# Kernel optimization log

Measured on AMD Instinct MI355X. Metric: run time of the kernel, lower is better.

The kernel has to match this reference:

```python
import jax, jax.numpy as jnp
import numpy as np

B, S, E, H = 2, 2048, 2048, 16
D = E // H  # head_dim = 128
ROPE_BASE = 10000.0


def _rope_tables(seq_len, dim, dtype):
    inv_freq = 1.0 / (ROPE_BASE ** (jnp.arange(0, dim, 2, dtype=jnp.float32) / dim))
    pos = jnp.arange(seq_len, dtype=jnp.float32)
    freqs = jnp.outer(pos, inv_freq)            # [S, D/2]
    emb = jnp.concatenate([freqs, freqs], -1)    # [S, D]
    return jnp.cos(emb).astype(dtype), jnp.sin(emb).astype(dtype)


def _rotate_half(x):
    x1, x2 = jnp.split(x, 2, axis=-1)
    return jnp.concatenate([-x2, x1], axis=-1)


def _apply_rope(x, cos, sin):
    # x: [B,H,S,D]; cos/sin: [S,D] broadcast over batch+heads
    return x * cos[None, None] + _rotate_half(x) * sin[None, None]


def setup_inputs() -> dict:
    key = jax.random.key(0)
    k1, k2, k3 = jax.random.split(key, 3)
    x = jax.random.normal(k1, (B, S, E), dtype=jnp.float32)
    w_qkv = jax.random.normal(k2, (3 * E, E), dtype=jnp.float32) * (E ** -0.5)
    w_out = jax.random.normal(k3, (E, E), dtype=jnp.float32) * (E ** -0.5)
    return {"x": x, "w_qkv": w_qkv, "w_out": w_out}


def reference(x, w_qkv, w_out):
    b, s, e = x.shape
    qkv = x @ w_qkv.T                                # [B,S,3E]
    q, k, v = jnp.split(qkv, 3, axis=-1)
    def to_heads(t):
        return t.reshape(b, s, H, D).transpose(0, 2, 1, 3)  # [B,H,S,D]
    q, k, v = to_heads(q), to_heads(k), to_heads(v)
    cos, sin = _rope_tables(s, D, x.dtype)
    q = _apply_rope(q, cos, sin)
    k = _apply_rope(k, cos, sin)
    scale = 1.0 / jnp.sqrt(jnp.asarray(D, x.dtype))
    scores = jnp.einsum('bhqd,bhkd->bhqk', q, k) * scale
    causal = jnp.tril(jnp.ones((s, s), dtype=bool))
    scores = jnp.where(causal[None, None], scores, jnp.asarray(-jnp.inf, scores.dtype))
    attn = jax.nn.softmax(scores, axis=-1)
    y = jnp.einsum('bhqk,bhkd->bhqd', attn, v)       # [B,H,S,D]
    y = y.transpose(0, 2, 1, 3).reshape(b, s, e)
    return y @ w_out.T
```

## Files before the change

### kernel.cpp

```cpp
#include <hip/hip_runtime.h>
#include <stdint.h>

constexpr int BATCH = 2;
constexpr int SEQ   = 2048;
constexpr int EMB   = 2048;
constexpr int NH    = 16;
constexpr int HD    = 128;
constexpr int QKV3  = 3 * EMB;

typedef unsigned short u16;
typedef __attribute__((ext_vector_type(8))) short bf16x8;
typedef __attribute__((ext_vector_type(4))) float floatx4;

__device__ inline float bf2f(u16 u) {
  union { unsigned int i; float f; } v; v.i = ((unsigned int)u) << 16; return v.f;
}
__device__ inline u16 f2bf(float f) {
  union { float f; unsigned int i; } v; v.f = f;
  unsigned int x = v.i;
  return (u16)((x + 0x7fffu + ((x >> 16) & 1u)) >> 16);
}

__device__ inline void load_lds16(const void* g, void* l) {
  __builtin_amdgcn_global_load_lds((const __attribute__((address_space(1))) unsigned int*)g,
                                   (__attribute__((address_space(3))) unsigned int*)l,
                                   16, 0, 0);
}

__device__ inline void block_barrier() {
  __builtin_amdgcn_sched_barrier(0);
  asm volatile("" ::: "memory");
  __builtin_amdgcn_s_barrier();
  asm volatile("" ::: "memory");
  __builtin_amdgcn_sched_barrier(0);
}

__global__ void cvt_f32_bf16(const float* __restrict__ src, u16* __restrict__ dst, int n4) {
  const int i = blockIdx.x * blockDim.x + threadIdx.x;
  if (i < n4) {
    const float4 v = ((const float4*)src)[i];
    ushort4 o;
    o.x = f2bf(v.x); o.y = f2bf(v.y); o.z = f2bf(v.z); o.w = f2bf(v.w);
    ((ushort4*)dst)[i] = o;
  }
}

constexpr int BM = 128, BN = 128, BK = 32;

template <bool F32OUT>
__global__ __launch_bounds__(256) void gemm_bt(const u16* __restrict__ A,
                                               const u16* __restrict__ Bm,
                                               u16* __restrict__ Cb,
                                               float* __restrict__ Cf,
                                               int M, int N, int K) {
  __shared__ __align__(16) u16 As[BM * BK];
  __shared__ __align__(16) u16 Bs[BN * BK];
  const int tid  = threadIdx.x;
  const int wave = tid >> 6, lane = tid & 63;
  const int wm = (wave & 1) * 64, wn = (wave >> 1) * 64;
  const int m0 = blockIdx.y * BM, n0 = blockIdx.x * BN;

  floatx4 acc[4][4];
#pragma unroll
  for (int i = 0; i < 4; ++i)
#pragma unroll
    for (int j = 0; j < 4; ++j) acc[i][j] = {0.f, 0.f, 0.f, 0.f};

  const int lrow = lane >> 2;
  const int lcol = (lane & 3) * 8;
  const int frow = lane & 15;
  const int fk   = (lane >> 4) * 8;

  for (int kt = 0; kt < K; kt += BK) {
#pragma unroll
    for (int inst = 0; inst < 2; ++inst) {
      const int rbase = wave * 32 + inst * 16;
      load_lds16(A  + (size_t)(m0 + rbase + lrow) * K + kt + lcol, &As[rbase * BK]);
      load_lds16(Bm + (size_t)(n0 + rbase + lrow) * K + kt + lcol, &Bs[rbase * BK]);
    }
    asm volatile("s_waitcnt vmcnt(0)" ::: "memory");
    __syncthreads();

    bf16x8 af[4], bfr[4];
#pragma unroll
    for (int mi = 0; mi < 4; ++mi)
      af[mi] = *(const bf16x8*)&As[(wm + mi * 16 + frow) * BK + fk];
#pragma unroll
    for (int ni = 0; ni < 4; ++ni)
      bfr[ni] = *(const bf16x8*)&Bs[(wn + ni * 16 + frow) * BK + fk];
#pragma unroll
    for (int mi = 0; mi < 4; ++mi)
#pragma unroll
      for (int ni = 0; ni < 4; ++ni)
        acc[mi][ni] = __builtin_amdgcn_mfma_f32_16x16x32_bf16(af[mi], bfr[ni], acc[mi][ni], 0, 0, 0);
    __syncthreads();
  }

  const int crow0 = (lane >> 4) * 4;
  const int ccol  = lane & 15;
#pragma unroll
  for (int mi = 0; mi < 4; ++mi)
#pragma unroll
    for (int ni = 0; ni < 4; ++ni) {
      const int row = m0 + wm + mi * 16 + crow0;
      const int col = n0 + wn + ni * 16 + ccol;
#pragma unroll
      for (int r = 0; r < 4; ++r) {
        const size_t off = (size_t)(row + r) * N + col;
        if (F32OUT) Cf[off] = acc[mi][ni][r];
        else        Cb[off] = f2bf(acc[mi][ni][r]);
      }
    }
}

__global__ __launch_bounds__(512, 2) void gemm_bt192(const u16* __restrict__ A,
                                                     const u16* __restrict__ Bm,
                                                     u16* __restrict__ Cb,
                                                     int M, int N, int K) {
  __shared__ __align__(16) u16 sh[57344];
  char* ldsb = (char*)sh;

  const int tid  = threadIdx.x;
  const int wave = tid >> 6, lane = tid & 63;
  const int wrow = wave >> 1;
  const int wcol = wave & 1;
  const int m0 = blockIdx.y * 256, n0 = blockIdx.x * 192;
  const int frow = lane & 15, quad = lane >> 4;
  const int KT = K >> 6;

  const int srow8 = tid >> 3;
  const int scolE = (((tid & 7) ^ (srow8 & 7)) << 3);
  auto stageA = [&](int t, int d, int a) {
    const int r = a * 64 + srow8;
    load_lds16(A + (size_t)(m0 + r) * K + t * 64 + scolE,
               ldsb + d * 57344 + a * 8192 + wave * 1024);
  };
  auto stageB = [&](int t, int d, int bi) {
    const int r = bi * 64 + srow8;
    load_lds16(Bm + (size_t)(n0 + r) * K + t * 64 + scolE,
               ldsb + d * 57344 + 32768 + bi * 8192 + wave * 1024);
  };

  floatx4 acc[4][6];
#pragma unroll
  for (int i = 0; i < 4; ++i)
#pragma unroll
    for (int j = 0; j < 6; ++j) acc[i][j] = {0.f, 0.f, 0.f, 0.f};

#pragma unroll
  for (int a = 0; a < 4; ++a) stageA(0, 0, a);
#pragma unroll
  for (int bi = 0; bi < 3; ++bi) stageB(0, 0, bi);

  for (int t = 0; t < KT; ++t) {
    const int d = t & 1, dn = d ^ 1;
    const char* dbuf = ldsb + d * 57344;
    const bool pf = (t + 1 < KT);

    if (pf) {
      stageA(t + 1, dn, 0); stageA(t + 1, dn, 1); stageA(t + 1, dn, 2);
      asm volatile("s_waitcnt vmcnt(3)" ::: "memory");
    } else {
      asm volatile("s_waitcnt vmcnt(0)" ::: "memory");
    }
    block_barrier();

    bf16x8 af[4][2], bf0[2][2];
#pragma unroll
    for (int mi = 0; mi < 4; ++mi) {
      const int ra = wrow * 64 + mi * 16 + frow;
#pragma unroll
      for (int kk = 0; kk < 2; ++kk) {
        const int cb = (kk * 64 + quad * 16) ^ ((ra & 7) << 4);
        af[mi][kk] = *(const bf16x8*)(dbuf + ra * 128 + cb);
      }
    }
#pragma unroll
    for (int ni = 0; ni < 2; ++ni) {
      const int rb = wcol * 96 + ni * 16 + frow;
#pragma unroll
      for (int kk = 0; kk < 2; ++kk) {
        const int cb = (kk * 64 + quad * 16) ^ ((rb & 7) << 4);
        bf0[ni][kk] = *(const bf16x8*)(dbuf + 32768 + rb * 128 + cb);
      }
    }
    asm volatile("s_waitcnt lgkmcnt(0)" ::: "memory");
    __builtin_amdgcn_sched_barrier(0);
    __builtin_amdgcn_s_setprio(1);
#pragma unroll
    for (int mi = 0; mi < 4; ++mi)
#pragma unroll
      for (int ni = 0; ni < 2; ++ni)
#pragma unroll
        for (int kk = 0; kk < 2; ++kk)
          acc[mi][ni] = __builtin_amdgcn_mfma_f32_16x16x32_bf16(af[mi][kk], bf0[ni][kk], acc[mi][ni], 0, 0, 0);
    __builtin_amdgcn_s_setprio(0);
    block_barrier();

    bf16x8 bf1[2][2];
#pragma unroll
    for (int ni = 0; ni < 2; ++ni) {
      const int rb = wcol * 96 + (2 + ni) * 16 + frow;
#pragma unroll
      for (int kk = 0; kk < 2; ++kk) {
        const int cb = (kk * 64 + quad * 16) ^ ((rb & 7) << 4);
        bf1[ni][kk] = *(const bf16x8*)(dbuf + 32768 + rb * 128 + cb);
      }
    }
    if (pf) { stageA(t + 1, dn, 3); stageB(t + 1, dn, 0); }
    block_barrier();
    asm volatile("s_waitcnt lgkmcnt(0)" ::: "memory");
    __builtin_amdgcn_sched_barrier(0);
    __builtin_amdgcn_s_setprio(1);
#pragma unroll
    for (int mi = 0; mi < 4; ++mi)
#pragma unroll
      for (int ni = 0; ni < 2; ++ni)
#pragma unroll
        for (int kk = 0; kk < 2; ++kk)
          acc[mi][2 + ni] = __builtin_amdgcn_mfma_f32_16x16x32_bf16(af[mi][kk], bf1[ni][kk], acc[mi][2 + ni], 0, 0, 0);
    __builtin_amdgcn_s_setprio(0);
    block_barrier();

    bf16x8 bf2[2][2];
#pragma unroll
    for (int ni = 0; ni < 2; ++ni) {
      const int rb = wcol * 96 + (4 + ni) * 16 + frow;
#pragma unroll
      for (int kk = 0; kk < 2; ++kk) {
        const int cb = (kk * 64 + quad * 16) ^ ((rb & 7) << 4);
        bf2[ni][kk] = *(const bf16x8*)(dbuf + 32768 + rb * 128 + cb);
      }
    }
    if (pf) { stageB(t + 1, dn, 1); stageB(t + 1, dn, 2); }
    block_barrier();
    asm volatile("s_waitcnt lgkmcnt(0)" ::: "memory");
    __builtin_amdgcn_sched_barrier(0);
    __builtin_amdgcn_s_setprio(1);
#pragma unroll
    for (int mi = 0; mi < 4; ++mi)
#pragma unroll
      for (int ni = 0; ni < 2; ++ni)
#pragma unroll
        for (int kk = 0; kk < 2; ++kk)
          acc[mi][4 + ni] = __builtin_amdgcn_mfma_f32_16x16x32_bf16(af[mi][kk], bf2[ni][kk], acc[mi][4 + ni], 0, 0, 0);
    __builtin_amdgcn_s_setprio(0);
    block_barrier();
  }

#pragma unroll
  for (int mi = 0; mi < 4; ++mi)
#pragma unroll
    for (int ni = 0; ni < 6; ++ni) {
      const int row = m0 + wrow * 64 + mi * 16 + quad * 4;
      const int col = n0 + wcol * 96 + ni * 16 + frow;
#pragma unroll
      for (int r = 0; r < 4; ++r)
        Cb[(size_t)(row + r) * N + col] = f2bf(acc[mi][ni][r]);
    }
}

__global__ void rope_inplace(u16* __restrict__ qkv) {
  const int t   = blockIdx.x * blockDim.x + threadIdx.x;
  const int j   = t & 63;
  const int idx = t >> 6;
  const int h   = idx & (NH - 1);
  const int bs  = idx >> 4;
  const int s   = bs & (SEQ - 1);

  u16* base = qkv + (size_t)bs * QKV3 + h * HD;

  const float inv_freq = exp2f(-(float)j * (13.287712379549449f / 64.0f));
  const float ang = (float)s * inv_freq;
  const float c = cosf(ang), sn = sinf(ang);

#pragma unroll
  for (int part = 0; part < 2; ++part) {
    u16* p = base + part * EMB;
    const float x1 = bf2f(p[j]), x2 = bf2f(p[j + 64]);
    p[j]      = f2bf(x1 * c - x2 * sn);
    p[j + 64] = f2bf(x2 * c + x1 * sn);
  }
}

__global__ __launch_bounds__(256) void transpose_v(const u16* __restrict__ qkv,
                                                   u16* __restrict__ VT) {
  __shared__ u16 vtile[64][136];
  const int tid = threadIdx.x;
  const int s0 = blockIdx.x * 64;
  const int bh = blockIdx.y;
  const int b = bh >> 4, h = bh & 15;

  const u16* Vp = qkv + (size_t)b * SEQ * QKV3 + 2 * EMB + h * HD;
  {
    const int r = tid >> 2, cp = (tid & 3) * 32;
    const uint4* src = (const uint4*)(Vp + (size_t)(s0 + r) * QKV3 + cp);
    uint4* dst = (uint4*)&vtile[r][cp];
    dst[0] = src[0]; dst[1] = src[1]; dst[2] = src[2]; dst[3] = src[3];
  }
  __syncthreads();
  {
    const int d = tid >> 1, ck = (tid & 1) * 32;
    ushort4 o[8];
#pragma unroll
    for (int i = 0; i < 8; ++i) {
      o[i].x = vtile[ck + i * 4 + 0][d];
      o[i].y = vtile[ck + i * 4 + 1][d];
      o[i].z = vtile[ck + i * 4 + 2][d];
      o[i].w = vtile[ck + i * 4 + 3][d];
    }
    ushort4* dst = (ushort4*)(VT + ((size_t)bh * HD + d) * SEQ + s0 + ck);
#pragma unroll
    for (int i = 0; i < 8; ++i) dst[i] = o[i];
  }
}

constexpr int PSTR = 72;

__global__ __launch_bounds__(256, 2) void attn_mfma(const u16* __restrict__ qkv,
                                                    const u16* __restrict__ VT,
                                                    u16* __restrict__ Y) {
  __shared__ __align__(16) u16 kb[2][64 * 128];
  __shared__ __align__(16) u16 vb[2][64 * 128];
  __shared__ __align__(16) u16 p_sh[4][16][PSTR];

  const int tid  = threadIdx.x;
  const int wave = tid >> 6, lane = tid & 63;
  const int bid  = blockIdx.x;
  const int bh   = bid & 31;
  const int pc   = bid >> 5;
  const int cq   = (pc < 8) ? pc : 23 - pc;
  const int qa   = cq;
  const int qb   = 31 - cq;
  const int b = bh >> 4, h = bh & 15;

  const u16* Qp  = qkv + (size_t)b * SEQ * QKV3 + h * HD;
  const u16* Kp  = Qp + EMB;
  const u16* VTp = VT + (size_t)bh * HD * SEQ;

  const int NT = 32 - cq;

  u16* kbf = &kb[0][0];

  {
    const int rl  = lane >> 4;
    const int cbp = (lane & 15) * 16;
#pragma unroll
    for (int i = 0; i < 8; ++i) {
      const int cc = wave * 8 + i;
      const int r  = cc * 4 + rl;
      const int gq = (r < 64) ? (qa * 64 + r) : (qb * 64 + r - 64);
      const int cbl = cbp ^ ((r & 7) << 4);
      load_lds16(Qp + (size_t)gq * QKV3 + (cbl >> 1), kbf + cc * 512);
    }
  }
  asm volatile("s_waitcnt vmcnt(0)" ::: "memory");
  block_barrier();

  const int frow = lane & 15;
  const int quad = lane >> 4;

  bf16x8 aq[2][4];
#pragma unroll
  for (int m = 0; m < 2; ++m)
#pragma unroll
    for (int ks = 0; ks < 4; ++ks) {
      const int qr = m * 64 + wave * 16 + frow;
      const int cb = (ks * 64 + quad * 16) ^ ((qr & 7) << 4);
      aq[m][ks] = *(const bf16x8*)((const char*)kbf + qr * 256 + cb);
    }
  asm volatile("s_waitcnt lgkmcnt(0)" ::: "memory");
  block_barrier();

  auto stage_k = [&](int t, int sel) {
    const int rl  = lane >> 4;
    const int cbp = (lane & 15) * 16;
#pragma unroll
    for (int i = 0; i < 4; ++i) {
      const int cc = wave * 4 + i;
      const int r  = cc * 4 + rl;
      const int cbl = cbp ^ ((r & 7) << 4);
      load_lds16(Kp + (size_t)(t * 64 + r) * QKV3 + (cbl >> 1), &kb[sel][cc * 512]);
    }
  };
  auto stage_v = [&](int t, int sel) {
    const int rl  = lane >> 3;
    const int cbp = (lane & 7) * 16;
#pragma unroll
    for (int i = 0; i < 4; ++i) {
      const int cc = wave * 4 + i;
      const int r  = cc * 8 + rl;
      const int cbl = cbp ^ ((r & 7) << 4);
      load_lds16(VTp + (size_t)r * SEQ + t * 64 + (cbl >> 1), &vb[sel][cc * 512]);
    }
  };

  floatx4 o_acc[2][8];
#pragma unroll
  for (int m = 0; m < 2; ++m)
#pragma unroll
    for (int dt = 0; dt < 8; ++dt) o_acc[m][dt] = {0.f, 0.f, 0.f, 0.f};
  float l_r[2][4];
#pragma unroll
  for (int m = 0; m < 2; ++m)
#pragma unroll
    for (int r = 0; r < 4; ++r) l_r[m][r] = 0.f;

  const float scale = 0.08838834764831845f;
  const float M0s   = 3.5355339059327378f;

  stage_k(0, 0);
  stage_v(0, 0);

  for (int t = 0; t < NT; ++t) {
    block_barrier();
    const bool havek = (t + 1 < NT);
    if (havek) {
      stage_k(t + 1, (t + 1) & 1);
      stage_v(t + 1, (t + 1) & 1);
      asm volatile("s_waitcnt vmcnt(8)" ::: "memory");
    } else {
      asm volatile("s_waitcnt vmcnt(0)" ::: "memory");
    }
    block_barrier();

    const char* kbuf = (const char*)&kb[t & 1][0];
    const char* vbuf = (const char*)&vb[t & 1][0];
    const bool aAct = (t <= qa);

    floatx4 s4[2][4];
    __builtin_amdgcn_s_setprio(1);
    if (aAct) {
#pragma unroll
      for (int nt = 0; nt < 4; ++nt) {
        floatx4 a0 = {0.f, 0.f, 0.f, 0.f}, a1 = {0.f, 0.f, 0.f, 0.f};
#pragma unroll
        for (int ks = 0; ks < 4; ++ks) {
          const int kr = nt * 16 + frow;
          const int cb = (ks * 64 + quad * 16) ^ ((kr & 7) << 4);
          const bf16x8 bk = *(const bf16x8*)(kbuf + kr * 256 + cb);
          a0 = __builtin_amdgcn_mfma_f32_16x16x32_bf16(aq[0][ks], bk, a0, 0, 0, 0);
          a1 = __builtin_amdgcn_mfma_f32_16x16x32_bf16(aq[1][ks], bk, a1, 0, 0, 0);
        }
        s4[0][nt] = a0; s4[1][nt] = a1;
      }
    } else {
#pragma unroll
      for (int nt = 0; nt < 4; ++nt) {
        floatx4 a1 = {0.f, 0.f, 0.f, 0.f};
#pragma unroll
        for (int ks = 0; ks < 4; ++ks) {
          const int kr = nt * 16 + frow;
          const int cb = (ks * 64 + quad * 16) ^ ((kr & 7) << 4);
          const bf16x8 bk = *(const bf16x8*)(kbuf + kr * 256 + cb);
          a1 = __builtin_amdgcn_mfma_f32_16x16x32_bf16(aq[1][ks], bk, a1, 0, 0, 0);
        }
        s4[1][nt] = a1;
      }
    }
    __builtin_amdgcn_s_setprio(0);

#pragma unroll
    for (int m = 0; m < 2; ++m) {
      if (m == 0 && !aAct) continue;
      const int tdiag = (m == 0) ? qa : qb;
      if (t == tdiag) {
#pragma unroll
        for (int nt = 0; nt < 4; ++nt)
#pragma unroll
          for (int r = 0; r < 4; ++r) {
            const int key = t * 64 + nt * 16 + frow;
            const int qg  = tdiag * 64 + wave * 16 + quad * 4 + r;
            if (key > qg) s4[m][nt][r] = -1.0e30f;
          }
      }
#pragma unroll
      for (int nt = 0; nt < 4; ++nt)
#pragma unroll
        for (int r = 0; r < 4; ++r)
          s4[m][nt][r] = __expf(fmaf(s4[m][nt][r], scale, -M0s));
#pragma unroll
      for (int r = 0; r < 4; ++r)
        l_r[m][r] += (s4[m][0][r] + s4[m][1][r]) + (s4[m][2][r] + s4[m][3][r]);
    }

    __builtin_amdgcn_s_setprio(1);
#pragma unroll
    for (int m = 0; m < 2; ++m) {
      if (m == 0 && !aAct) continue;
#pragma unroll
      for (int nt = 0; nt < 4; ++nt)
#pragma unroll
        for (int r = 0; r < 4; ++r)
          p_sh[wave][quad * 4 + r][nt * 16 + frow] = f2bf(s4[m][nt][r]);
#pragma unroll
      for (int step = 0; step < 2; ++step) {
        const bf16x8 ap = *(const bf16x8*)&p_sh[wave][frow][step * 32 + quad * 8];
#pragma unroll
        for (int dt = 0; dt < 8; ++dt) {
          const int vr = dt * 16 + frow;
          const int cb = (step * 64 + quad * 16) ^ ((vr & 7) << 4);
          const bf16x8 bv = *(const bf16x8*)(vbuf + vr * 128 + cb);
          o_acc[m][dt] = __builtin_amdgcn_mfma_f32_16x16x32_bf16(ap, bv, o_acc[m][dt], 0, 0, 0);
        }
      }
    }
    __builtin_amdgcn_s_setprio(0);
  }

#pragma unroll
  for (int off = 1; off <= 8; off <<= 1)
#pragma unroll
    for (int m = 0; m < 2; ++m)
#pragma unroll
      for (int r = 0; r < 4; ++r) l_r[m][r] += __shfl_xor(l_r[m][r], off);

#pragma unroll
  for (int m = 0; m < 2; ++m) {
    const int qbase = ((m == 0) ? qa : qb) * 64 + wave * 16;
    float invl[4];
#pragma unroll
    for (int r = 0; r < 4; ++r) invl[r] = 1.f / l_r[m][r];
#pragma unroll
    for (int dt = 0; dt < 8; ++dt)
#pragma unroll
      for (int r = 0; r < 4; ++r) {
        const int qg = qbase + quad * 4 + r;
        const size_t off = ((size_t)b * SEQ + qg) * EMB + h * HD + dt * 16 + frow;
        Y[off] = f2bf(o_acc[m][dt][r] * invl[r]);
      }
  }
}

extern "C" void kernel_launch(void* const* d_in, const int* in_sizes, int n_in,
                              void* d_out, int out_size, void* d_ws, size_t ws_size,
                              hipStream_t stream) {
  const float* x_f     = (const float*)d_in[0];
  const float* w_qkv_f = (const float*)d_in[1];
  const float* w_out_f = (const float*)d_in[2];
  float* out = (float*)d_out;

  const int M = BATCH * SEQ;
  const size_t n_x    = (size_t)M * EMB;
  const size_t n_wqkv = (size_t)3 * EMB * EMB;
  const size_t n_wout = (size_t)EMB * EMB;

  u16* xb    = (u16*)d_ws;
  u16* wqkvb = xb + n_x;
  u16* qkv   = wqkvb + n_wqkv;
  u16* VT    = qkv + (size_t)M * QKV3;
  u16* woutb = wqkvb;
  u16* Yb    = xb;

  cvt_f32_bf16<<<(int)((n_x / 4 + 255) / 256), 256, 0, stream>>>(x_f, xb, (int)(n_x / 4));
  cvt_f32_bf16<<<(int)((n_wqkv / 4 + 255) / 256), 256, 0, stream>>>(w_qkv_f, wqkvb, (int)(n_wqkv / 4));

  gemm_bt192<<<dim3(QKV3 / 192, M / 256), 512, 0, stream>>>(
      xb, wqkvb, qkv, M, QKV3, EMB);

  rope_inplace<<<(BATCH * SEQ * NH * 64) / 256, 256, 0, stream>>>(qkv);
  transpose_v<<<dim3(SEQ / 64, BATCH * NH), 256, 0, stream>>>(qkv, VT);

  cvt_f32_bf16<<<(int)((n_wout / 4 + 255) / 256), 256, 0, stream>>>(w_out_f, woutb, (int)(n_wout / 4));

  attn_mfma<<<dim3((SEQ / 128) * BATCH * NH), 256, 0, stream>>>(qkv, VT, Yb);

  gemm_bt<true><<<dim3(EMB / BN, M / BM), 256, 0, stream>>>(
      Yb, woutb, nullptr, out, M, EMB, EMB);
}
```

Before: 377.7 us.

## Add pipelined 256x128 GEMM for output projection and restructure QKV GEMM prefetch

Replaces the simple single-buffered 128x128 output-projection GEMM with a new 512-thread, double-buffered, swizzled-LDS kernel that has a 256x128 tile and writes fp32 output. The QKV GEMM main loop is also reworked. All next-tile loads are now issued at the top of each iteration, and the B fragment reads are interleaved with MFMA groups using partial lgkmcnt waits. This drops several block barriers per iteration. The aim is better overlap of global loads, LDS reads and MFMA work, with fewer synchronisations. The cost is higher register pressure from holding all fragments at once.

Result: faster. 362.9 us (-3.9%).

```diff
diff --git a/kernel.cpp b/kernel.cpp
--- a/kernel.cpp
+++ b/kernel.cpp
@@ -45,74 +45,6 @@
   }
 }
 
-constexpr int BM = 128, BN = 128, BK = 32;
-
-template <bool F32OUT>
-__global__ __launch_bounds__(256) void gemm_bt(const u16* __restrict__ A,
-                                               const u16* __restrict__ Bm,
-                                               u16* __restrict__ Cb,
-                                               float* __restrict__ Cf,
-                                               int M, int N, int K) {
-  __shared__ __align__(16) u16 As[BM * BK];
-  __shared__ __align__(16) u16 Bs[BN * BK];
-  const int tid  = threadIdx.x;
-  const int wave = tid >> 6, lane = tid & 63;
-  const int wm = (wave & 1) * 64, wn = (wave >> 1) * 64;
-  const int m0 = blockIdx.y * BM, n0 = blockIdx.x * BN;
-
-  floatx4 acc[4][4];
-#pragma unroll
-  for (int i = 0; i < 4; ++i)
-#pragma unroll
-    for (int j = 0; j < 4; ++j) acc[i][j] = {0.f, 0.f, 0.f, 0.f};
-
-  const int lrow = lane >> 2;
-  const int lcol = (lane & 3) * 8;
-  const int frow = lane & 15;
-  const int fk   = (lane >> 4) * 8;
-
-  for (int kt = 0; kt < K; kt += BK) {
-#pragma unroll
-    for (int inst = 0; inst < 2; ++inst) {
-      const int rbase = wave * 32 + inst * 16;
-      load_lds16(A  + (size_t)(m0 + rbase + lrow) * K + kt + lcol, &As[rbase * BK]);
-      load_lds16(Bm + (size_t)(n0 + rbase + lrow) * K + kt + lcol, &Bs[rbase * BK]);
-    }
-    asm volatile("s_waitcnt vmcnt(0)" ::: "memory");
-    __syncthreads();
-
-    bf16x8 af[4], bfr[4];
-#pragma unroll
-    for (int mi = 0; mi < 4; ++mi)
-      af[mi] = *(const bf16x8*)&As[(wm + mi * 16 + frow) * BK + fk];
-#pragma unroll
-    for (int ni = 0; ni < 4; ++ni)
-      bfr[ni] = *(const bf16x8*)&Bs[(wn + ni * 16 + frow) * BK + fk];
-#pragma unroll
-    for (int mi = 0; mi < 4; ++mi)
-#pragma unroll
-      for (int ni = 0; ni < 4; ++ni)
-        acc[mi][ni] = __builtin_amdgcn_mfma_f32_16x16x32_bf16(af[mi], bfr[ni], acc[mi][ni], 0, 0, 0);
-    __syncthreads();
-  }
-
-  const int crow0 = (lane >> 4) * 4;
-  const int ccol  = lane & 15;
-#pragma unroll
-  for (int mi = 0; mi < 4; ++mi)
-#pragma unroll
-    for (int ni = 0; ni < 4; ++ni) {
-      const int row = m0 + wm + mi * 16 + crow0;
-      const int col = n0 + wn + ni * 16 + ccol;
-#pragma unroll
-      for (int r = 0; r < 4; ++r) {
-        const size_t off = (size_t)(row + r) * N + col;
-        if (F32OUT) Cf[off] = acc[mi][ni][r];
-        else        Cb[off] = f2bf(acc[mi][ni][r]);
-      }
-    }
-}
-
 __global__ __launch_bounds__(512, 2) void gemm_bt192(const u16* __restrict__ A,
                                                      const u16* __restrict__ Bm,
                                                      u16* __restrict__ Cb,
@@ -130,16 +62,20 @@
 
   const int srow8 = tid >> 3;
   const int scolE = (((tid & 7) ^ (srow8 & 7)) << 3);
-  auto stageA = [&](int t, int d, int a) {
-    const int r = a * 64 + srow8;
-    load_lds16(A + (size_t)(m0 + r) * K + t * 64 + scolE,
-               ldsb + d * 57344 + a * 8192 + wave * 1024);
+  auto stageT = [&](int t, int d) {
+#pragma unroll
+    for (int a = 0; a < 4; ++a) {
+      const int r = a * 64 + srow8;
+      load_lds16(A + (size_t)(m0 + r) * K + t * 64 + scolE,
+                 ldsb + d * 57344 + a * 8192 + wave * 1024);
+    }
+#pragma unroll
+    for (int bi = 0; bi < 3; ++bi) {
+      const int r = bi * 64 + srow8;
+      load_lds16(Bm + (size_t)(n0 + r) * K + t * 64 + scolE,
+                 ldsb + d * 57344 + 32768 + bi * 8192 + wave * 1024);
+    }
   };
-  auto stageB = [&](int t, int d, int bi) {
-    const int r = bi * 64 + srow8;
-    load_lds16(Bm + (size_t)(n0 + r) * K + t * 64 + scolE,
-               ldsb + d * 57344 + 32768 + bi * 8192 + wave * 1024);
-  };
 
   floatx4 acc[4][6];
 #pragma unroll
@@ -147,25 +83,22 @@
 #pragma unroll
     for (int j = 0; j < 6; ++j) acc[i][j] = {0.f, 0.f, 0.f, 0.f};
 
-#pragma unroll
-  for (int a = 0; a < 4; ++a) stageA(0, 0, a);
-#pragma unroll
-  for (int bi = 0; bi < 3; ++bi) stageB(0, 0, bi);
+  stageT(0, 0);
 
   for (int t = 0; t < KT; ++t) {
     const int d = t & 1, dn = d ^ 1;
     const char* dbuf = ldsb + d * 57344;
-    const bool pf = (t + 1 < KT);
-
-    if (pf) {
-      stageA(t + 1, dn, 0); stageA(t + 1, dn, 1); stageA(t + 1, dn, 2);
-      asm volatile("s_waitcnt vmcnt(3)" ::: "memory");
+
+    block_barrier();
+    if (t + 1 < KT) {
+      stageT(t + 1, dn);
+      asm volatile("s_waitcnt vmcnt(7)" ::: "memory");
     } else {
       asm volatile("s_waitcnt vmcnt(0)" ::: "memory");
     }
     block_barrier();
 
-    bf16x8 af[4][2], bf0[2][2];
+    bf16x8 af[4][2], bf0[2][2], bf1[2][2], bf2[2][2];
 #pragma unroll
     for (int mi = 0; mi < 4; ++mi) {
       const int ra = wrow * 64 + mi * 16 + frow;
@@ -184,6 +117,48 @@
         bf0[ni][kk] = *(const bf16x8*)(dbuf + 32768 + rb * 128 + cb);
       }
     }
+#pragma unroll
+    for (int ni = 0; ni < 2; ++ni) {
+      const int rb = wcol * 96 + (2 + ni) * 16 + frow;
+#pragma unroll
+      for (int kk = 0; kk < 2; ++kk) {
+        const int cb = (kk * 64 + quad * 16) ^ ((rb & 7) << 4);
+        bf1[ni][kk] = *(const bf16x8*)(dbuf + 32768 + rb * 128 + cb);
+      }
+    }
+    asm volatile("s_waitcnt lgkmcnt(4)" ::: "memory");
+    __builtin_amdgcn_sched_barrier(0);
+    __builtin_amdgcn_s_setprio(1);
+#pragma unroll
+    for (int mi = 0; mi < 4; ++mi)
+#pragma unroll
+      for (int ni = 0; ni < 2; ++ni)
+#pragma unroll
+        for (int kk = 0; kk < 2; ++kk)
+          acc[mi][ni] = __builtin_amdgcn_mfma_f32_16x16x32_bf16(af[mi][kk], bf0[ni][kk], acc[mi][ni], 0, 0, 0);
+    __builtin_amdgcn_s_setprio(0);
+
+#pragma unroll
+    for (int ni = 0; ni < 2; ++ni) {
+      const int rb = wcol * 96 + (4 + ni) * 16 + frow;
+#pragma unroll
+      for (int kk = 0; kk < 2; ++kk) {
+        const int cb = (kk * 64 + quad * 16) ^ ((rb & 7) << 4);
+        bf2[ni][kk] = *(const bf16x8*)(dbuf + 32768 + rb * 128 + cb);
+      }
+    }
+    asm volatile("s_waitcnt lgkmcnt(4)" ::: "memory");
+    __builtin_amdgcn_sched_barrier(0);
+    __builtin_amdgcn_s_setprio(1);
+#pragma unroll
+    for (int mi = 0; mi < 4; ++mi)
+#pragma unroll
+      for (int ni = 0; ni < 2; ++ni)
+#pragma unroll
+        for (int kk = 0; kk < 2; ++kk)
+          acc[mi][2 + ni] = __builtin_amdgcn_mfma_f32_16x16x32_bf16(af[mi][kk], bf1[ni][kk], acc[mi][2 + ni], 0, 0, 0);
+    __builtin_amdgcn_s_setprio(0);
+
     asm volatile("s_waitcnt lgkmcnt(0)" ::: "memory");
     __builtin_amdgcn_sched_barrier(0);
     __builtin_amdgcn_s_setprio(1);
@@ -193,22 +168,115 @@
       for (int ni = 0; ni < 2; ++ni)
 #pragma unroll
         for (int kk = 0; kk < 2; ++kk)
-          acc[mi][ni] = __builtin_amdgcn_mfma_f32_16x16x32_bf16(af[mi][kk], bf0[ni][kk], acc[mi][ni], 0, 0, 0);
+          acc[mi][4 + ni] = __builtin_amdgcn_mfma_f32_16x16x32_bf16(af[mi][kk], bf2[ni][kk], acc[mi][4 + ni], 0, 0, 0);
     __builtin_amdgcn_s_setprio(0);
+  }
+
+#pragma unroll
+  for (int mi = 0; mi < 4; ++mi)
+#pragma unroll
+    for (int ni = 0; ni < 6; ++ni) {
+      const int row = m0 + wrow * 64 + mi * 16 + quad * 4;
+      const int col = n0 + wcol * 96 + ni * 16 + frow;
+#pragma unroll
+      for (int r = 0; r < 4; ++r)
+        Cb[(size_t)(row + r) * N + col] = f2bf(acc[mi][ni][r]);
+    }
+}
+
+__global__ __launch_bounds__(512, 2) void gemm_bt128f(const u16* __restrict__ A,
+                                                      const u16* __restrict__ Bm,
+                                                      float* __restrict__ Cf,
+                                                      int M, int N, int K) {
+  __shared__ __align__(16) u16 sh[49152];
+  char* ldsb = (char*)sh;
+
+  const int tid  = threadIdx.x;
+  const int wave = tid >> 6, lane = tid & 63;
+  const int wrow = wave >> 1;
+  const int wcol = wave & 1;
+  const int m0 = blockIdx.y * 256, n0 = blockIdx.x * 128;
+  const int frow = lane & 15, quad = lane >> 4;
+  const int KT = K >> 6;
+
+  const int srow8 = tid >> 3;
+  const int scolE = (((tid & 7) ^ (srow8 & 7)) << 3);
+  auto stageT = [&](int t, int d) {
+#pragma unroll
+    for (int a = 0; a < 4; ++a) {
+      const int r = a * 64 + srow8;
+      load_lds16(A + (size_t)(m0 + r) * K + t * 64 + scolE,
+                 ldsb + d * 49152 + a * 8192 + wave * 1024);
+    }
+#pragma unroll
+    for (int bi = 0; bi < 2; ++bi) {
+      const int r = bi * 64 + srow8;
+      load_lds16(Bm + (size_t)(n0 + r) * K + t * 64 + scolE,
+                 ldsb + d * 49152 + 32768 + bi * 8192 + wave * 1024);
+    }
+  };
+
+  floatx4 acc[4][4];
+#pragma unroll
+  for (int i = 0; i < 4; ++i)
+#pragma unroll
+    for (int j = 0; j < 4; ++j) acc[i][j] = {0.f, 0.f, 0.f, 0.f};
+
+  stageT(0, 0);
+
+  for (int t = 0; t < KT; ++t) {
+    const int d = t & 1, dn = d ^ 1;
+    const char* dbuf = ldsb + d * 49152;
+
     block_barrier();
-
-    bf16x8 bf1[2][2];
+    if (t + 1 < KT) {
+      stageT(t + 1, dn);
+      asm volatile("s_waitcnt vmcnt(6)" ::: "memory");
+    } else {
+      asm volatile("s_waitcnt vmcnt(0)" ::: "memory");
+    }
+    block_barrier();
+
+    bf16x8 af[4][2], bf0[2][2], bf1[2][2];
+#pragma unroll
+    for (int mi = 0; mi < 4; ++mi) {
+      const int ra = wrow * 64 + mi * 16 + frow;
+#pragma unroll
+      for (int kk = 0; kk < 2; ++kk) {
+        const int cb = (kk * 64 + quad * 16) ^ ((ra & 7) << 4);
+        af[mi][kk] = *(const bf16x8*)(dbuf + ra * 128 + cb);
+      }
+    }
 #pragma unroll
     for (int ni = 0; ni < 2; ++ni) {
-      const int rb = wcol * 96 + (2 + ni) * 16 + frow;
+      const int rb = wcol * 64 + ni * 16 + frow;
+#pragma unroll
+      for (int kk = 0; kk < 2; ++kk) {
+        const int cb = (kk * 64 + quad * 16) ^ ((rb & 7) << 4);
+        bf0[ni][kk] = *(const bf16x8*)(dbuf + 32768 + rb * 128 + cb);
+      }
+    }
+#pragma unroll
+    for (int ni = 0; ni < 2; ++ni) {
+      const int rb = wcol * 64 + (2 + ni) * 16 + frow;
 #pragma unroll
       for (int kk = 0; kk < 2; ++kk) {
         const int cb = (kk * 64 + quad * 16) ^ ((rb & 7) << 4);
         bf1[ni][kk] = *(const bf16x8*)(dbuf + 32768 + rb * 128 + cb);
       }
     }
-    if (pf) { stageA(t + 1, dn, 3); stageB(t + 1, dn, 0); }
-    block_barrier();
+    asm volatile("s_waitcnt lgkmcnt(4)" ::: "memory");
+    __builtin_amdgcn_sched_barrier(0);
+    __builtin_amdgcn_s_setprio(1);
+#pragma unroll
+    for (int mi = 0; mi < 4; ++mi)
+#pragma unroll
+      for (int ni = 0; ni < 2; ++ni)
+#pragma unroll
+        for (int kk = 0; kk < 2; ++kk)
+          acc[mi][ni] = __builtin_amdgcn_mfma_f32_16x16x32_bf16(af[mi][kk], bf0[ni][kk], acc[mi][ni], 0, 0, 0);
+    __builtin_amdgcn_s_setprio(0);
+
     asm volatile("s_waitcnt lgkmcnt(0)" ::: "memory");
     __builtin_amdgcn_sched_barrier(0);
     __builtin_amdgcn_s_setprio(1);
@@ -220,43 +288,17 @@
         for (int kk = 0; kk < 2; ++kk)
           acc[mi][2 + ni] = __builtin_amdgcn_mfma_f32_16x16x32_bf16(af[mi][kk], bf1[ni][kk], acc[mi][2 + ni], 0, 0, 0);
     __builtin_amdgcn_s_setprio(0);
-    block_barrier();
-
-    bf16x8 bf2[2][2];
-#pragma unroll
-    for (int ni = 0; ni < 2; ++ni) {
-      const int rb = wcol * 96 + (4 + ni) * 16 + frow;
-#pragma unroll
-      for (int kk = 0; kk < 2; ++kk) {
-        const int cb = (kk * 64 + quad * 16) ^ ((rb & 7) << 4);
-        bf2[ni][kk] = *(const bf16x8*)(dbuf + 32768 + rb * 128 + cb);
-      }
-    }
-    if (pf) { stageB(t + 1, dn, 1); stageB(t + 1, dn, 2); }
-    block_barrier();
-    asm volatile("s_waitcnt lgkmcnt(0)" ::: "memory");
-    __builtin_amdgcn_sched_barrier(0);
-    __builtin_amdgcn_s_setprio(1);
-#pragma unroll
-    for (int mi = 0; mi < 4; ++mi)
-#pragma unroll
-      for (int ni = 0; ni < 2; ++ni)
-#pragma unroll
-        for (int kk = 0; kk < 2; ++kk)
-          acc[mi][4 + ni] = __builtin_amdgcn_mfma_f32_16x16x32_bf16(af[mi][kk], bf2[ni][kk], acc[mi][4 + ni], 0, 0, 0);
-    __builtin_amdgcn_s_setprio(0);
-    block_barrier();
   }
 
 #pragma unroll
   for (int mi = 0; mi < 4; ++mi)
 #pragma unroll
-    for (int ni = 0; ni < 6; ++ni) {
+    for (int ni = 0; ni < 4; ++ni) {
       const int row = m0 + wrow * 64 + mi * 16 + quad * 4;
-      const int col = n0 + wcol * 96 + ni * 16 + frow;
+      const int col = n0 + wcol * 64 + ni * 16 + frow;
 #pragma unroll
       for (int r = 0; r < 4; ++r)
-        Cb[(size_t)(row + r) * N + col] = f2bf(acc[mi][ni][r]);
+        Cf[(size_t)(row + r) * N + col] = acc[mi][ni][r];
     }
 }
 
@@ -565,6 +607,6 @@
 
   attn_mfma<<<dim3((SEQ / 128) * BATCH * NH), 256, 0, stream>>>(qkv, VT, Yb);
 
-  gemm_bt<true><<<dim3(EMB / BN, M / BM), 256, 0, stream>>>(
-      Yb, woutb, nullptr, out, M, EMB, EMB);
-}
+  gemm_bt128f<<<dim3(EMB / 128, M / 256), 512, 0, stream>>>(
+      Yb, woutb, out, M, EMB, EMB);
+}
```
